# Performance work log

Measured on AMD Instinct MI355X. Metric: run time of the kernel, lower is better.

The kernel has to match this reference:

```python
import jax, jax.numpy as jnp
import numpy as np

EMBED_DIM = 1024
NUM_HEADS = 16
HEAD_DIM = EMBED_DIM // NUM_HEADS
STD = 0.02


def setup_inputs() -> dict:
    key = jax.random.key(0)
    k1, k2, k3 = jax.random.split(key, 3)
    B, S = 2, 2048
    inputs = jax.random.normal(k1, (B, S, EMBED_DIM), dtype=jnp.float32)
    # qkv projection: Linear(E, 3E); torch Linear weight is [out, in]
    w_qkv = jax.random.normal(k2, (3 * EMBED_DIM, EMBED_DIM), dtype=jnp.float32) * STD
    b_qkv = jnp.zeros((3 * EMBED_DIM,), dtype=jnp.float32)
    w_out = jax.random.normal(k3, (EMBED_DIM, EMBED_DIM), dtype=jnp.float32) * STD
    b_out = jnp.zeros((EMBED_DIM,), dtype=jnp.float32)
    return {"inputs": inputs, "w_qkv": w_qkv, "b_qkv": b_qkv, "w_out": w_out, "b_out": b_out}


def reference(inputs, w_qkv, b_qkv, w_out, b_out):
    B, S, E = inputs.shape
    qkv = inputs @ w_qkv.T + b_qkv                      # [B,S,3E]
    q, k, v = jnp.split(qkv, 3, axis=2)                 # each [B,S,E]

    def split_heads(t):
        return t.reshape(B, S, NUM_HEADS, HEAD_DIM).transpose(0, 2, 1, 3)  # [B,H,S,D]

    q, k, v = split_heads(q), split_heads(k), split_heads(v)
    scores = jnp.einsum('bhqd,bhkd->bhqk', q, k) * (1.0 / np.sqrt(HEAD_DIM))
    causal = jnp.tril(jnp.ones((S, S), dtype=bool))     # [S,S]
    scores = jnp.where(causal[None, None, :, :], scores, -jnp.inf)
    probs = jax.nn.softmax(scores, axis=-1)             # dropout is identity in eval mode
    ctx = jnp.einsum('bhqk,bhkd->bhqd', probs, v)       # [B,H,S,D]
    ctx = ctx.transpose(0, 2, 1, 3).reshape(B, S, E)
    return ctx @ w_out.T + b_out
```

## Files before the change

kernel.cpp:

```cpp
#include <hip/hip_runtime.h>
#include <hip/hip_bf16.h>

#define BATCH 2
#define SEQ   2048
#define EMB   1024
#define NHEAD 16
#define HDIM  64
#define MTOT  (BATCH*SEQ)
#define KTOT  EMB

#define NX  (MTOT*EMB)
#define NW1 (3*EMB*EMB)
#define NW2 (EMB*EMB)
#define NCVT (NX+NW1+NW2)

typedef short bf8 __attribute__((ext_vector_type(8)));
typedef short s4v __attribute__((ext_vector_type(4)));
typedef float f4  __attribute__((ext_vector_type(4)));
typedef unsigned int uint;

__device__ __forceinline__ short f2b(float f) {
    __hip_bfloat16 h = __float2bfloat16(f);
    return __builtin_bit_cast(short, h);
}
__device__ __forceinline__ void gl_lds16(const short* g, short* l) {
    __builtin_amdgcn_global_load_lds(
        (const __attribute__((address_space(1))) uint*)g,
        (__attribute__((address_space(3))) uint*)l, 16, 0, 0);
}
#define SWZ_SRC(lane)      ((((lane) ^ ((lane)>>2) ^ ((lane)>>4)) & 3) * 8)
#define SWZ_RD(quad, l16)  ((((quad) ^ (l16) ^ ((l16)>>2)) & 3) * 8)

__global__ __launch_bounds__(256) void cvt_all(
    const float* __restrict__ X, const float* __restrict__ W1,
    const float* __restrict__ W2,
    short* __restrict__ xb, short* __restrict__ w1b, short* __restrict__ w2b)
{
    int i4 = (blockIdx.x * 256 + threadIdx.x) * 4;
    const float* src; short* dst; int off;
    if (i4 < NX)            { src = X;  dst = xb;  off = i4; }
    else if (i4 < NX + NW1) { src = W1; dst = w1b; off = i4 - NX; }
    else                    { src = W2; dst = w2b; off = i4 - NX - NW1; }
    float4 v = *(const float4*)&src[off];
    s4v o; o[0]=f2b(v.x); o[1]=f2b(v.y); o[2]=f2b(v.z); o[3]=f2b(v.w);
    *(s4v*)&dst[off] = o;
}

__global__ __launch_bounds__(256) void gemm_qkv(
    const short* __restrict__ Xb, const short* __restrict__ Wb,
    const float* __restrict__ bias,
    short* __restrict__ qb, short* __restrict__ kb, short* __restrict__ vtb)
{
    __shared__ __align__(16) short As[2*128*32];
    __shared__ __align__(16) short Bs[2*128*32];
    const int tid  = threadIdx.x;
    const int lane = tid & 63;
    const int w    = tid >> 6;
    const int l16  = lane & 15, quad = lane >> 4;
    const int wm   = (w >> 1) * 64, wn = (w & 1) * 64;
    const int srow = (lane >> 2);
    const int scol = SWZ_SRC(lane);
    f4 acc[4][4] = {};
    for (int k0 = 0; k0 < KTOT; k0 += 64) {
        #pragma unroll
        for (int t = 0; t < 4; t++) {
            const int rr = w*32 + (t & 1)*16;
            const int kc = t >> 1;
            int ra = blockIdx.x*128 + rr + srow;
            gl_lds16(&Xb[(size_t)ra*KTOT + k0 + kc*32 + scol], &As[kc*4096 + rr*32]);
            int rb = blockIdx.y*128 + rr + srow;
            gl_lds16(&Wb[(size_t)rb*KTOT + k0 + kc*32 + scol], &Bs[kc*4096 + rr*32]);
        }
        __syncthreads();
        #pragma unroll
        for (int kc = 0; kc < 2; kc++) {
            bf8 af[4], bf[4];
            #pragma unroll
            for (int t = 0; t < 4; t++) {
                af[t] = *(const bf8*)&As[kc*4096 + (wm + t*16 + l16)*32 + SWZ_RD(quad, l16)];
                bf[t] = *(const bf8*)&Bs[kc*4096 + (wn + t*16 + l16)*32 + SWZ_RD(quad, l16)];
            }
            #pragma unroll
            for (int mt = 0; mt < 4; mt++)
                #pragma unroll
                for (int nt = 0; nt < 4; nt++)
                    acc[mt][nt] = __builtin_amdgcn_mfma_f32_16x16x32_bf16(af[mt], bf[nt], acc[mt][nt], 0, 0, 0);
        }
        __syncthreads();
    }
    #pragma unroll
    for (int mt = 0; mt < 4; mt++)
    #pragma unroll
    for (int nt = 0; nt < 4; nt++) {
        int colg = blockIdx.y*128 + wn + nt*16 + l16;
        float bv = bias[colg];
        #pragma unroll
        for (int r = 0; r < 4; r++) {
            int rowg = blockIdx.x*128 + wm + mt*16 + quad*4 + r;
            short h = f2b(acc[mt][nt][r] + bv);
            int bb = rowg >> 11, s = rowg & 2047;
            if (colg < 1024) {
                int hh = colg >> 6, d = colg & 63;
                qb[(((bb*NHEAD + hh)*SEQ + s) << 6) + d] = h;
            } else if (colg < 2048) {
                int c2 = colg - 1024, hh = c2 >> 6, d = c2 & 63;
                kb[(((bb*NHEAD + hh)*SEQ + s) << 6) + d] = h;
            } else {
                int c3 = colg - 2048, hh = c3 >> 6, d = c3 & 63;
                int ssw = (s & ~63) | (((s & 15) << 2) | ((s >> 4) & 3));
                vtb[((bb*NHEAD + hh)*HDIM + d)*SEQ + ssw] = h;
            }
        }
    }
}

__global__ __launch_bounds__(256, 4) void attn(
    const short* __restrict__ qb, const short* __restrict__ kb,
    const short* __restrict__ vtb, short* __restrict__ ctx)
{
    __shared__ __align__(16) short Ks[2*4096];
    __shared__ __align__(16) short Vs[2*4096];
    __shared__ __align__(16) short pl[4][16*64];
    const int tid = threadIdx.x;
    const int w = tid >> 6, lane = tid & 63;
    const int l16 = lane & 15, quad = lane >> 4;
    const int f  = blockIdx.x;
    const int bh = f & 31;
    const int j5 = (f >> 5) & 7;
    const int hq = f >> 8;
    const int tq = (hq == 0) ? j5 : (hq == 1) ? (15 - j5)
                 : (hq == 2) ? (16 + j5) : (31 - j5);
    const int q0w = tq*64 + w*16;
    const int base = bh * (SEQ*HDIM);
    short* myp = pl[w];
    const float SC = 0.125f * 1.44269504f;

    const int lq  = lane >> 2;
    const int lsw = SWZ_SRC(lane);

    const bool isk = (w < 2);
    short* tb = isk ? Ks : Vs;
    const int sstep = isk ? 64*HDIM : 64;
    const short* sp0; const short* sp1; const short* sp2; const short* sp3;
    int dof[4];
    {
        const int wb2 = (w & 1) * 4;
        #pragma unroll
        for (int tt = 0; tt < 4; tt++) {
            int t = wb2 + tt, cc = t & 1, g = (t >> 1) & 3;
            dof[tt] = (cc*64 + g*16)*32;
            const short* s = isk ? &kb[base + (g*16 + lq)*HDIM + cc*32 + lsw]
                                 : &vtb[base + (g*16 + lq)*SEQ + cc*32 + lsw];
            if (tt == 0) sp0 = s; else if (tt == 1) sp1 = s;
            else if (tt == 2) sp2 = s; else sp3 = s;
        }
    }

    bf8 qa[2];
    #pragma unroll
    for (int kc = 0; kc < 2; kc++)
        qa[kc] = *(const bf8*)&qb[base + (q0w + l16)*HDIM + kc*32 + quad*8];

    f4 o[4] = {};
    float lacc[4] = {};
    const int rdK = l16*32 + SWZ_RD(quad, l16);

    gl_lds16(sp0, tb + dof[0]); gl_lds16(sp1, tb + dof[1]);
    gl_lds16(sp2, tb + dof[2]); gl_lds16(sp3, tb + dof[3]);
    sp0 += sstep; sp1 += sstep; sp2 += sstep; sp3 += sstep;
    __syncthreads();

    int buf = 0;
    for (int st = 0; st <= tq; st++) {
        if (st < tq) {
            short* d = tb + (buf ^ 1)*4096;
            gl_lds16(sp0, d + dof[0]); gl_lds16(sp1, d + dof[1]);
            gl_lds16(sp2, d + dof[2]); gl_lds16(sp3, d + dof[3]);
            sp0 += sstep; sp1 += sstep; sp2 += sstep; sp3 += sstep;
        }
        const int kbase = buf*4096 + rdK;
        f4 s[4] = {};
        #pragma unroll
        for (int kf = 0; kf < 4; kf++)
            #pragma unroll
            for (int c = 0; c < 2; c++) {
                bf8 kfr = *(const bf8*)&Ks[kbase + (c*64 + kf*16)*32];
                s[kf] = __builtin_amdgcn_mfma_f32_16x16x32_bf16(qa[c], kfr, s[kf], 0, 0, 0);
            }
        if (st == tq) {
            const int j0 = st*64;
            #pragma unroll
            for (int r = 0; r < 4; r++) {
                const int row = quad*4 + r;
                const int qi  = q0w + row;
                float e[4];
                #pragma unroll
                for (int kf = 0; kf < 4; kf++) {
                    e[kf] = __builtin_amdgcn_exp2f(s[kf][r] * SC);
                    if (j0 + kf*16 + l16 > qi) e[kf] = 0.0f;
                    lacc[r] += e[kf];
                }
                uint u01 = __builtin_amdgcn_perm(__builtin_bit_cast(uint, e[1]),
                                                 __builtin_bit_cast(uint, e[0]), 0x07060302u);
                uint u23 = __builtin_amdgcn_perm(__builtin_bit_cast(uint, e[3]),
                                                 __builtin_bit_cast(uint, e[2]), 0x07060302u);
                uint2 pk = {u01, u23};
                int c8 = ((l16 >> 1) ^ (row & 7));
                *(uint2*)&myp[row*64 + c8*8 + (l16 & 1)*4] = pk;
            }
        } else {
            #pragma unroll
            for (int r = 0; r < 4; r++) {
                const int row = quad*4 + r;
                float e[4];
                #pragma unroll
                for (int kf = 0; kf < 4; kf++) {
                    e[kf] = __builtin_amdgcn_exp2f(s[kf][r] * SC);
                    lacc[r] += e[kf];
                }
                uint u01 = __builtin_amdgcn_perm(__builtin_bit_cast(uint, e[1]),
                                                 __builtin_bit_cast(uint, e[0]), 0x07060302u);
                uint u23 = __builtin_amdgcn_perm(__builtin_bit_cast(uint, e[3]),
                                                 __builtin_bit_cast(uint, e[2]), 0x07060302u);
                uint2 pk = {u01, u23};
                int c8 = ((l16 >> 1) ^ (row & 7));
                *(uint2*)&myp[row*64 + c8*8 + (l16 & 1)*4] = pk;
            }
        }
        asm volatile("" ::: "memory");
        bf8 pa[2];
        #pragma unroll
        for (int kc = 0; kc < 2; kc++)
            pa[kc] = *(const bf8*)&myp[l16*64 + (((kc*4 + quad) ^ (l16 & 7)))*8];
        #pragma unroll
        for (int dt = 0; dt < 4; dt++)
            #pragma unroll
            for (int c = 0; c < 2; c++) {
                bf8 vf = *(const bf8*)&Vs[kbase + (c*64 + dt*16)*32];
                o[dt] = __builtin_amdgcn_mfma_f32_16x16x32_bf16(pa[c], vf, o[dt], 0, 0, 0);
            }
        __syncthreads();
        buf ^= 1;
    }
    #pragma unroll
    for (int r = 0; r < 4; r++) {
        float v = lacc[r];
        v += __shfl_xor(v, 1);
        v += __shfl_xor(v, 2);
        v += __shfl_xor(v, 4);
        v += __shfl_xor(v, 8);
        lacc[r] = v;
    }
    const int b = bh >> 4, h = bh & 15;
    #pragma unroll
    for (int r = 0; r < 4; r++) {
        float inv = 1.0f / lacc[r];
        int qi = q0w + quad*4 + r;
        int rowoff = (b*SEQ + qi)*EMB + h*HDIM;
        #pragma unroll
        for (int dt = 0; dt < 4; dt++)
            ctx[rowoff + dt*16 + l16] = f2b(o[dt][r] * inv);
    }
}

__global__ __launch_bounds__(256) void gemm_out(
    const short* __restrict__ A, const short* __restrict__ Wb,
    const float* __restrict__ bias, float* __restrict__ out)
{
    __shared__ __align__(16) short As[2*64*32];
    __shared__ __align__(16) short Bs[2*64*32];
    const int f = blockIdx.x;
    const int xcd = f & 7, i = f >> 3;
    const int by = xcd*2 + (i & 1);
    const int bx = i >> 1;
    const int tid  = threadIdx.x;
    const int lane = tid & 63;
    const int w    = tid >> 6;
    const int l16  = lane & 15, quad = lane >> 4;
    const int wm   = (w >> 1) * 32, wn = (w & 1) * 32;
    const int srow = (lane >> 2);
    const int scol = SWZ_SRC(lane);
    f4 acc[2][2] = {};
    for (int k0 = 0; k0 < KTOT; k0 += 64) {
        #pragma unroll
        for (int kc = 0; kc < 2; kc++) {
            int ra = bx*64 + w*16 + srow;
            gl_lds16(&A[(size_t)ra*KTOT + k0 + kc*32 + scol],  &As[kc*2048 + (w*16)*32]);
            int rb = by*64 + w*16 + srow;
            gl_lds16(&Wb[(size_t)rb*KTOT + k0 + kc*32 + scol], &Bs[kc*2048 + (w*16)*32]);
        }
        __syncthreads();
        #pragma unroll
        for (int kc = 0; kc < 2; kc++) {
            bf8 af[2], bf[2];
            #pragma unroll
            for (int t = 0; t < 2; t++) {
                af[t] = *(const bf8*)&As[kc*2048 + (wm + t*16 + l16)*32 + SWZ_RD(quad, l16)];
                bf[t] = *(const bf8*)&Bs[kc*2048 + (wn + t*16 + l16)*32 + SWZ_RD(quad, l16)];
            }
            #pragma unroll
            for (int mt = 0; mt < 2; mt++)
                #pragma unroll
                for (int nt = 0; nt < 2; nt++)
                    acc[mt][nt] = __builtin_amdgcn_mfma_f32_16x16x32_bf16(af[mt], bf[nt], acc[mt][nt], 0, 0, 0);
        }
        __syncthreads();
    }
    #pragma unroll
    for (int mt = 0; mt < 2; mt++)
    #pragma unroll
    for (int nt = 0; nt < 2; nt++) {
        int colg = by*64 + wn + nt*16 + l16;
        float bv = bias[colg];
        #pragma unroll
        for (int r = 0; r < 4; r++) {
            int rowg = bx*64 + wm + mt*16 + quad*4 + r;
            out[(size_t)rowg*EMB + colg] = acc[mt][nt][r] + bv;
        }
    }
}

extern "C" void kernel_launch(void* const* d_in, const int* in_sizes, int n_in,
                              void* d_out, int out_size, void* d_ws, size_t ws_size,
                              hipStream_t stream) {
    const float* X    = (const float*)d_in[0];
    const float* Wqkv = (const float*)d_in[1];
    const float* Bqkv = (const float*)d_in[2];
    const float* Wout = (const float*)d_in[3];
    const float* Bout = (const float*)d_in[4];
    float* out = (float*)d_out;

    short* xb    = (short*)d_ws;
    short* w1b   = xb  + NX;
    short* w2b   = w1b + NW1;
    short* qb    = w2b + NW2;
    short* kb    = qb  + NX;
    short* vtb   = kb  + NX;
    short* ctx   = vtb + NX;

    cvt_all<<<NCVT/1024, 256, 0, stream>>>(X, Wqkv, Wout, xb, w1b, w2b);
    dim3 g1(MTOT/128, 3*EMB/128);
    gemm_qkv<<<g1, 256, 0, stream>>>(xb, w1b, Bqkv, qb, kb, vtb);
    attn<<<dim3(1024), 256, 0, stream>>>(qb, kb, vtb, ctx);
    gemm_out<<<dim3(1024), 256, 0, stream>>>(ctx, w2b, Bout, out);
}
```

Measured before the change: 176.8 us.

## Double-buffer LDS in both GEMMs and retile QKV GEMM to 256x192 blocks

Both projection GEMMs now double-buffer their LDS tiles. The next K-slice's global-to-LDS loads are issued before computing on the current slice, and one barrier per iteration is removed. The QKV GEMM grows from 128x128 tiles with 256 threads to 256x192 tiles with 512 threads and 8x3 MFMA accumulators per wave, launched as a 1D grid of 256 blocks with an XCD-aware block remap. This aims to hide load latency and raise data reuse, at the cost of more LDS and registers per block and a grid that may fill the CUs unevenly.

```diff
diff --git a/kernel.cpp b/kernel.cpp
--- a/kernel.cpp
+++ b/kernel.cpp
@@ -46,69 +46,101 @@
     *(s4v*)&dst[off] = o;
 }
 
-__global__ __launch_bounds__(256) void gemm_qkv(
+__global__ __launch_bounds__(512, 2) void gemm_qkv(
     const short* __restrict__ Xb, const short* __restrict__ Wb,
     const float* __restrict__ bias,
     short* __restrict__ qb, short* __restrict__ kb, short* __restrict__ vtb)
 {
-    __shared__ __align__(16) short As[2*128*32];
-    __shared__ __align__(16) short Bs[2*128*32];
+    __shared__ __align__(16) short As[2*2*256*32];
+    __shared__ __align__(16) short Bs[2*2*192*32];
     const int tid  = threadIdx.x;
     const int lane = tid & 63;
     const int w    = tid >> 6;
     const int l16  = lane & 15, quad = lane >> 4;
-    const int wm   = (w >> 1) * 64, wn = (w & 1) * 64;
-    const int srow = (lane >> 2);
+    const int wm   = (w >> 2) * 128;
+    const int wn   = (w & 3) * 48;
+    const int srow = lane >> 2;
     const int scol = SWZ_SRC(lane);
-    f4 acc[4][4] = {};
-    for (int k0 = 0; k0 < KTOT; k0 += 64) {
-        #pragma unroll
-        for (int t = 0; t < 4; t++) {
-            const int rr = w*32 + (t & 1)*16;
-            const int kc = t >> 1;
-            int ra = blockIdx.x*128 + rr + srow;
-            gl_lds16(&Xb[(size_t)ra*KTOT + k0 + kc*32 + scol], &As[kc*4096 + rr*32]);
-            int rb = blockIdx.y*128 + rr + srow;
-            gl_lds16(&Wb[(size_t)rb*KTOT + k0 + kc*32 + scol], &Bs[kc*4096 + rr*32]);
+
+    const int id  = blockIdx.x;
+    const int sid = (id & 7) * 32 + (id >> 3);
+    const int bm  = sid >> 4, bn = sid & 15;
+    const int row0 = bm * 256, col0 = bn * 192;
+
+    const short* pa[4]; int da[4];
+    #pragma unroll
+    for (int j = 0; j < 4; j++) {
+        int idx = j*8 + w, kc = idx & 1, g = idx >> 1;
+        pa[j] = &Xb[(size_t)(row0 + g*16 + srow)*KTOT + kc*32 + scol];
+        da[j] = (kc*256 + g*16) * 32;
+    }
+    const short* pb[3]; int db[3];
+    #pragma unroll
+    for (int j = 0; j < 3; j++) {
+        int idx = j*8 + w, kc = idx & 1, g = idx >> 1;
+        pb[j] = &Wb[(size_t)(col0 + g*16 + srow)*KTOT + kc*32 + scol];
+        db[j] = (kc*192 + g*16) * 32;
+    }
+
+    f4 acc[8][3] = {};
+
+    #pragma unroll
+    for (int j = 0; j < 4; j++) gl_lds16(pa[j], &As[da[j]]);
+    #pragma unroll
+    for (int j = 0; j < 3; j++) gl_lds16(pb[j], &Bs[db[j]]);
+    __syncthreads();
+
+    for (int t = 0; t < 16; t++) {
+        const int buf = t & 1;
+        if (t < 15) {
+            const int boA = (buf ^ 1) * 16384;
+            const int boB = (buf ^ 1) * 12288;
+            const int ko  = (t + 1) * 64;
+            #pragma unroll
+            for (int j = 0; j < 4; j++) gl_lds16(pa[j] + ko, &As[boA + da[j]]);
+            #pragma unroll
+            for (int j = 0; j < 3; j++) gl_lds16(pb[j] + ko, &Bs[boB + db[j]]);
+        }
+        const int ab = buf * 16384, bb = buf * 12288;
+        #pragma unroll
+        for (int kc = 0; kc < 2; kc++) {
+            bf8 af[8], bf[3];
+            #pragma unroll
+            for (int m = 0; m < 8; m++)
+                af[m] = *(const bf8*)&As[ab + (kc*256 + wm + m*16 + l16)*32 + SWZ_RD(quad, l16)];
+            #pragma unroll
+            for (int n = 0; n < 3; n++)
+                bf[n] = *(const bf8*)&Bs[bb + (kc*192 + wn + n*16 + l16)*32 + SWZ_RD(quad, l16)];
+            #pragma unroll
+            for (int m = 0; m < 8; m++)
+                #pragma unroll
+                for (int n = 0; n < 3; n++)
+                    acc[m][n] = __builtin_amdgcn_mfma_f32_16x16x32_bf16(af[m], bf[n], acc[m][n], 0, 0, 0);
         }
         __syncthreads();
-        #pragma unroll
-        for (int kc = 0; kc < 2; kc++) {
-            bf8 af[4], bf[4];
-            #pragma unroll
-            for (int t = 0; t < 4; t++) {
-                af[t] = *(const bf8*)&As[kc*4096 + (wm + t*16 + l16)*32 + SWZ_RD(quad, l16)];
-                bf[t] = *(const bf8*)&Bs[kc*4096 + (wn + t*16 + l16)*32 + SWZ_RD(quad, l16)];
-            }
-            #pragma unroll
-            for (int mt = 0; mt < 4; mt++)
-                #pragma unroll
-                for (int nt = 0; nt < 4; nt++)
-                    acc[mt][nt] = __builtin_amdgcn_mfma_f32_16x16x32_bf16(af[mt], bf[nt], acc[mt][nt], 0, 0, 0);
-        }
-        __syncthreads();
-    }
-    #pragma unroll
-    for (int mt = 0; mt < 4; mt++)
-    #pragma unroll
-    for (int nt = 0; nt < 4; nt++) {
-        int colg = blockIdx.y*128 + wn + nt*16 + l16;
+    }
+
+    #pragma unroll
+    for (int m = 0; m < 8; m++)
+    #pragma unroll
+    for (int n = 0; n < 3; n++) {
+        int colg = col0 + wn + n*16 + l16;
         float bv = bias[colg];
         #pragma unroll
         for (int r = 0; r < 4; r++) {
-            int rowg = blockIdx.x*128 + wm + mt*16 + quad*4 + r;
-            short h = f2b(acc[mt][nt][r] + bv);
-            int bb = rowg >> 11, s = rowg & 2047;
+            int rowg = row0 + wm + m*16 + quad*4 + r;
+            short h = f2b(acc[m][n][r] + bv);
+            int bb2 = rowg >> 11, s = rowg & 2047;
             if (colg < 1024) {
                 int hh = colg >> 6, d = colg & 63;
-                qb[(((bb*NHEAD + hh)*SEQ + s) << 6) + d] = h;
+                qb[(((bb2*NHEAD + hh)*SEQ + s) << 6) + d] = h;
             } else if (colg < 2048) {
                 int c2 = colg - 1024, hh = c2 >> 6, d = c2 & 63;
-                kb[(((bb*NHEAD + hh)*SEQ + s) << 6) + d] = h;
+                kb[(((bb2*NHEAD + hh)*SEQ + s) << 6) + d] = h;
             } else {
                 int c3 = colg - 2048, hh = c3 >> 6, d = c3 & 63;
                 int ssw = (s & ~63) | (((s & 15) << 2) | ((s >> 4) & 3));
-                vtb[((bb*NHEAD + hh)*HDIM + d)*SEQ + ssw] = h;
+                vtb[((bb2*NHEAD + hh)*HDIM + d)*SEQ + ssw] = h;
             }
         }
     }
@@ -267,8 +299,8 @@
     const short* __restrict__ A, const short* __restrict__ Wb,
     const float* __restrict__ bias, float* __restrict__ out)
 {
-    __shared__ __align__(16) short As[2*64*32];
-    __shared__ __align__(16) short Bs[2*64*32];
+    __shared__ __align__(16) short As[2*2*64*32];
+    __shared__ __align__(16) short Bs[2*2*64*32];
     const int f = blockIdx.x;
     const int xcd = f & 7, i = f >> 3;
     const int by = xcd*2 + (i & 1);
@@ -280,23 +312,35 @@
     const int wm   = (w >> 1) * 32, wn = (w & 1) * 32;
     const int srow = (lane >> 2);
     const int scol = SWZ_SRC(lane);
+
+    const short* pa0 = &A [(size_t)(bx*64 + w*16 + srow)*KTOT + 0*32 + scol];
+    const short* pa1 = &A [(size_t)(bx*64 + w*16 + srow)*KTOT + 1*32 + scol];
+    const short* pb0 = &Wb[(size_t)(by*64 + w*16 + srow)*KTOT + 0*32 + scol];
+    const short* pb1 = &Wb[(size_t)(by*64 + w*16 + srow)*KTOT + 1*32 + scol];
+    const int d0 = (0*64 + w*16)*32, d1 = (1*64 + w*16)*32;
+
     f4 acc[2][2] = {};
-    for (int k0 = 0; k0 < KTOT; k0 += 64) {
-        #pragma unroll
-        for (int kc = 0; kc < 2; kc++) {
-            int ra = bx*64 + w*16 + srow;
-            gl_lds16(&A[(size_t)ra*KTOT + k0 + kc*32 + scol],  &As[kc*2048 + (w*16)*32]);
-            int rb = by*64 + w*16 + srow;
-            gl_lds16(&Wb[(size_t)rb*KTOT + k0 + kc*32 + scol], &Bs[kc*2048 + (w*16)*32]);
-        }
-        __syncthreads();
+
+    gl_lds16(pa0, &As[d0]); gl_lds16(pa1, &As[d1]);
+    gl_lds16(pb0, &Bs[d0]); gl_lds16(pb1, &Bs[d1]);
+    __syncthreads();
+
+    for (int t = 0; t < 16; t++) {
+        const int buf = t & 1;
+        if (t < 15) {
+            const int bo = (buf ^ 1) * 4096;
+            const int ko = (t + 1) * 64;
+            gl_lds16(pa0 + ko, &As[bo + d0]); gl_lds16(pa1 + ko, &As[bo + d1]);
+            gl_lds16(pb0 + ko, &Bs[bo + d0]); gl_lds16(pb1 + ko, &Bs[bo + d1]);
+        }
+        const int ab = buf * 4096;
         #pragma unroll
         for (int kc = 0; kc < 2; kc++) {
             bf8 af[2], bf[2];
             #pragma unroll
-            for (int t = 0; t < 2; t++) {
-                af[t] = *(const bf8*)&As[kc*2048 + (wm + t*16 + l16)*32 + SWZ_RD(quad, l16)];
-                bf[t] = *(const bf8*)&Bs[kc*2048 + (wn + t*16 + l16)*32 + SWZ_RD(quad, l16)];
+            for (int t2 = 0; t2 < 2; t2++) {
+                af[t2] = *(const bf8*)&As[ab + (kc*64 + wm + t2*16 + l16)*32 + SWZ_RD(quad, l16)];
+                bf[t2] = *(const bf8*)&Bs[ab + (kc*64 + wn + t2*16 + l16)*32 + SWZ_RD(quad, l16)];
             }
             #pragma unroll
             for (int mt = 0; mt < 2; mt++)
@@ -306,6 +350,7 @@
         }
         __syncthreads();
     }
+
     #pragma unroll
     for (int mt = 0; mt < 2; mt++)
     #pragma unroll
@@ -339,8 +384,7 @@
     short* ctx   = vtb + NX;
 
     cvt_all<<<NCVT/1024, 256, 0, stream>>>(X, Wqkv, Wout, xb, w1b, w2b);
-    dim3 g1(MTOT/128, 3*EMB/128);
-    gemm_qkv<<<g1, 256, 0, stream>>>(xb, w1b, Bqkv, qb, kb, vtb);
+    gemm_qkv<<<dim3(256), 512, 0, stream>>>(xb, w1b, Bqkv, qb, kb, vtb);
     attn<<<dim3(1024), 256, 0, stream>>>(qb, kb, vtb, ctx);
     gemm_out<<<dim3(1024), 256, 0, stream>>>(ctx, w2b, Bout, out);
 }
```

Result: slower. 190.7 us (+7.9%).

## Rewrite QKV GEMM as 256x256 tile, 8-wave double-buffered pipelined kernel

Applied to the files above, without the earlier changes.

The QKV projection GEMM moves from 128x128 tiles with 4 waves and a plain load-sync-compute loop to 256x256 tiles with 8 waves. Shared memory is double-buffered, and global-to-LDS loads for the next k-step are interleaved with four MFMA quadrants, using explicit vmcnt waits, raw barriers and s_setprio around the MFMA bursts. Block ids are remapped into groups so neighbouring blocks share rows and columns for L2 reuse. The aim is to hide memory latency and raise arithmetic intensity, at the cost of fewer blocks (192), higher register pressure and fragile hand-tuned waitcnt ordering.

```diff
diff --git a/kernel.cpp b/kernel.cpp
--- a/kernel.cpp
+++ b/kernel.cpp
@@ -30,6 +30,10 @@
 }
 #define SWZ_SRC(lane)      ((((lane) ^ ((lane)>>2) ^ ((lane)>>4)) & 3) * 8)
 #define SWZ_RD(quad, l16)  ((((quad) ^ (l16) ^ ((l16)>>2)) & 3) * 8)
+
+#define BARRIER() do { asm volatile("" ::: "memory"); \
+                       __builtin_amdgcn_s_barrier(); \
+                       asm volatile("" ::: "memory"); } while (0)
 
 __global__ __launch_bounds__(256) void cvt_all(
     const float* __restrict__ X, const float* __restrict__ W1,
@@ -46,69 +50,168 @@
     *(s4v*)&dst[off] = o;
 }
 
-__global__ __launch_bounds__(256) void gemm_qkv(
+__global__ __launch_bounds__(512, 1) void gemm_qkv(
     const short* __restrict__ Xb, const short* __restrict__ Wb,
     const float* __restrict__ bias,
     short* __restrict__ qb, short* __restrict__ kb, short* __restrict__ vtb)
 {
-    __shared__ __align__(16) short As[2*128*32];
-    __shared__ __align__(16) short Bs[2*128*32];
+    __shared__ __align__(16) short As[2*2*256*32];
+    __shared__ __align__(16) short Bs[2*2*256*32];
     const int tid  = threadIdx.x;
     const int lane = tid & 63;
     const int w    = tid >> 6;
     const int l16  = lane & 15, quad = lane >> 4;
-    const int wm   = (w >> 1) * 64, wn = (w & 1) * 64;
-    const int srow = (lane >> 2);
+    const int wh   = w >> 2;
+    const int wl   = w & 3;
+    const int wm   = wh * 128;
+    const int wn   = wl * 64;
+    const int srow = lane >> 2;
     const int scol = SWZ_SRC(lane);
-    f4 acc[4][4] = {};
-    for (int k0 = 0; k0 < KTOT; k0 += 64) {
-        #pragma unroll
-        for (int t = 0; t < 4; t++) {
-            const int rr = w*32 + (t & 1)*16;
-            const int kc = t >> 1;
-            int ra = blockIdx.x*128 + rr + srow;
-            gl_lds16(&Xb[(size_t)ra*KTOT + k0 + kc*32 + scol], &As[kc*4096 + rr*32]);
-            int rb = blockIdx.y*128 + rr + srow;
-            gl_lds16(&Wb[(size_t)rb*KTOT + k0 + kc*32 + scol], &Bs[kc*4096 + rr*32]);
-        }
-        __syncthreads();
+
+    const int id  = blockIdx.x;
+    const int x   = id & 7;
+    const int j   = id >> 3;
+    const int bmL = j / 6, bnL = j - bmL*6;
+    const int bm  = (x & 3)*4 + bmL;
+    const int bn  = (x >> 2)*6 + bnL;
+    const int row0 = bm * 256, col0 = bn * 256;
+
+    const short* pA0[2]; const short* pA1[2];
+    const short* pB0[2]; const short* pB1[2];
+    int dA0[2], dA1[2], dB0[2], dB1[2];
+    #pragma unroll
+    for (int kc = 0; kc < 2; kc++) {
+        int ra0 = wm + 0  + wl*16;
+        int ra1 = wm + 64 + wl*16;
+        int rb0 = wn + 0  + wh*16;
+        int rb1 = wn + 32 + wh*16;
+        pA0[kc] = &Xb[(size_t)(row0 + ra0 + srow)*KTOT + kc*32 + scol];
+        pA1[kc] = &Xb[(size_t)(row0 + ra1 + srow)*KTOT + kc*32 + scol];
+        pB0[kc] = &Wb[(size_t)(col0 + rb0 + srow)*KTOT + kc*32 + scol];
+        pB1[kc] = &Wb[(size_t)(col0 + rb1 + srow)*KTOT + kc*32 + scol];
+        dA0[kc] = kc*8192 + ra0*32;
+        dA1[kc] = kc*8192 + ra1*32;
+        dB0[kc] = kc*8192 + rb0*32;
+        dB1[kc] = kc*8192 + rb1*32;
+    }
+
+    f4 acc[8][4] = {};
+
+    gl_lds16(pA0[0], &As[dA0[0]]); gl_lds16(pA0[1], &As[dA0[1]]);
+    gl_lds16(pB0[0], &Bs[dB0[0]]); gl_lds16(pB0[1], &Bs[dB0[1]]);
+    gl_lds16(pB1[0], &Bs[dB1[0]]); gl_lds16(pB1[1], &Bs[dB1[1]]);
+    gl_lds16(pA1[0], &As[dA1[0]]); gl_lds16(pA1[1], &As[dA1[1]]);
+    asm volatile("s_waitcnt vmcnt(4)" ::: "memory");
+    BARRIER();
+
+    const int swz = SWZ_RD(quad, l16);
+    bf8 af[4][2], bf0[2][2], bf1[2][2];
+
+    for (int t = 0; t < 16; t++) {
+        const int ab = (t & 1) * 16384;
+        const int nb = ((t & 1) ^ 1) * 16384;
+        const int ko = (t + 1) * 64;
+
         #pragma unroll
         for (int kc = 0; kc < 2; kc++) {
-            bf8 af[4], bf[4];
-            #pragma unroll
-            for (int t = 0; t < 4; t++) {
-                af[t] = *(const bf8*)&As[kc*4096 + (wm + t*16 + l16)*32 + SWZ_RD(quad, l16)];
-                bf[t] = *(const bf8*)&Bs[kc*4096 + (wn + t*16 + l16)*32 + SWZ_RD(quad, l16)];
-            }
-            #pragma unroll
-            for (int mt = 0; mt < 4; mt++)
-                #pragma unroll
-                for (int nt = 0; nt < 4; nt++)
-                    acc[mt][nt] = __builtin_amdgcn_mfma_f32_16x16x32_bf16(af[mt], bf[nt], acc[mt][nt], 0, 0, 0);
-        }
-        __syncthreads();
-    }
-    #pragma unroll
-    for (int mt = 0; mt < 4; mt++)
-    #pragma unroll
-    for (int nt = 0; nt < 4; nt++) {
-        int colg = blockIdx.y*128 + wn + nt*16 + l16;
+            #pragma unroll
+            for (int m = 0; m < 4; m++)
+                af[m][kc] = *(const bf8*)&As[ab + kc*8192 + (wm + m*16 + l16)*32 + swz];
+            #pragma unroll
+            for (int n = 0; n < 2; n++)
+                bf0[n][kc] = *(const bf8*)&Bs[ab + kc*8192 + (wn + n*16 + l16)*32 + swz];
+        }
+        gl_lds16(pA0[0] + ko, &As[nb + dA0[0]]);
+        gl_lds16(pA0[1] + ko, &As[nb + dA0[1]]);
+        asm volatile("s_waitcnt vmcnt(4)" ::: "memory");
+        BARRIER();
+        __builtin_amdgcn_s_setprio(1);
+        #pragma unroll
+        for (int m = 0; m < 4; m++)
+            #pragma unroll
+            for (int n = 0; n < 2; n++)
+                #pragma unroll
+                for (int kc = 0; kc < 2; kc++)
+                    acc[m][n] = __builtin_amdgcn_mfma_f32_16x16x32_bf16(af[m][kc], bf0[n][kc], acc[m][n], 0, 0, 0);
+        __builtin_amdgcn_s_setprio(0);
+        BARRIER();
+
+        #pragma unroll
+        for (int kc = 0; kc < 2; kc++)
+            #pragma unroll
+            for (int n = 0; n < 2; n++)
+                bf1[n][kc] = *(const bf8*)&Bs[ab + kc*8192 + (wn + 32 + n*16 + l16)*32 + swz];
+        gl_lds16(pB0[0] + ko, &Bs[nb + dB0[0]]);
+        gl_lds16(pB0[1] + ko, &Bs[nb + dB0[1]]);
+        asm volatile("s_waitcnt vmcnt(4)" ::: "memory");
+        BARRIER();
+        __builtin_amdgcn_s_setprio(1);
+        #pragma unroll
+        for (int m = 0; m < 4; m++)
+            #pragma unroll
+            for (int n = 0; n < 2; n++)
+                #pragma unroll
+                for (int kc = 0; kc < 2; kc++)
+                    acc[m][2+n] = __builtin_amdgcn_mfma_f32_16x16x32_bf16(af[m][kc], bf1[n][kc], acc[m][2+n], 0, 0, 0);
+        __builtin_amdgcn_s_setprio(0);
+        BARRIER();
+
+        #pragma unroll
+        for (int kc = 0; kc < 2; kc++)
+            #pragma unroll
+            for (int m = 0; m < 4; m++)
+                af[m][kc] = *(const bf8*)&As[ab + kc*8192 + (wm + 64 + m*16 + l16)*32 + swz];
+        gl_lds16(pB1[0] + ko, &Bs[nb + dB1[0]]);
+        gl_lds16(pB1[1] + ko, &Bs[nb + dB1[1]]);
+        BARRIER();
+        __builtin_amdgcn_s_setprio(1);
+        #pragma unroll
+        for (int m = 0; m < 4; m++)
+            #pragma unroll
+            for (int n = 0; n < 2; n++)
+                #pragma unroll
+                for (int kc = 0; kc < 2; kc++)
+                    acc[4+m][2+n] = __builtin_amdgcn_mfma_f32_16x16x32_bf16(af[m][kc], bf1[n][kc], acc[4+m][2+n], 0, 0, 0);
+        __builtin_amdgcn_s_setprio(0);
+        BARRIER();
+
+        gl_lds16(pA1[0] + ko, &As[nb + dA1[0]]);
+        gl_lds16(pA1[1] + ko, &As[nb + dA1[1]]);
+        asm volatile("s_waitcnt vmcnt(4)" ::: "memory");
+        BARRIER();
+        __builtin_amdgcn_s_setprio(1);
+        #pragma unroll
+        for (int m = 0; m < 4; m++)
+            #pragma unroll
+            for (int n = 0; n < 2; n++)
+                #pragma unroll
+                for (int kc = 0; kc < 2; kc++)
+                    acc[4+m][n] = __builtin_amdgcn_mfma_f32_16x16x32_bf16(af[m][kc], bf0[n][kc], acc[4+m][n], 0, 0, 0);
+        __builtin_amdgcn_s_setprio(0);
+        BARRIER();
+    }
+
+    #pragma unroll
+    for (int m = 0; m < 8; m++)
+    #pragma unroll
+    for (int n = 0; n < 4; n++) {
+        int colg = col0 + wn + n*16 + l16;
         float bv = bias[colg];
         #pragma unroll
         for (int r = 0; r < 4; r++) {
-            int rowg = blockIdx.x*128 + wm + mt*16 + quad*4 + r;
-            short h = f2b(acc[mt][nt][r] + bv);
-            int bb = rowg >> 11, s = rowg & 2047;
+            int rowg = row0 + wm + m*16 + quad*4 + r;
+            short h = f2b(acc[m][n][r] + bv);
+            int bb2 = rowg >> 11, s = rowg & 2047;
             if (colg < 1024) {
                 int hh = colg >> 6, d = colg & 63;
-                qb[(((bb*NHEAD + hh)*SEQ + s) << 6) + d] = h;
+                qb[(((bb2*NHEAD + hh)*SEQ + s) << 6) + d] = h;
             } else if (colg < 2048) {
                 int c2 = colg - 1024, hh = c2 >> 6, d = c2 & 63;
-                kb[(((bb*NHEAD + hh)*SEQ + s) << 6) + d] = h;
+                kb[(((bb2*NHEAD + hh)*SEQ + s) << 6) + d] = h;
             } else {
                 int c3 = colg - 2048, hh = c3 >> 6, d = c3 & 63;
                 int ssw = (s & ~63) | (((s & 15) << 2) | ((s >> 4) & 3));
-                vtb[((bb*NHEAD + hh)*HDIM + d)*SEQ + ssw] = h;
+                vtb[((bb2*NHEAD + hh)*HDIM + d)*SEQ + ssw] = h;
             }
         }
     }
@@ -339,8 +442,7 @@
     short* ctx   = vtb + NX;
 
     cvt_all<<<NCVT/1024, 256, 0, stream>>>(X, Wqkv, Wout, xb, w1b, w2b);
-    dim3 g1(MTOT/128, 3*EMB/128);
-    gemm_qkv<<<g1, 256, 0, stream>>>(xb, w1b, Bqkv, qb, kb, vtb);
+    gemm_qkv<<<dim3(192), 512, 0, stream>>>(xb, w1b, Bqkv, qb, kb, vtb);
     attn<<<dim3(1024), 256, 0, stream>>>(qb, kb, vtb, ctx);
     gemm_out<<<dim3(1024), 256, 0, stream>>>(ctx, w2b, Bout, out);
 }
```

Result: slower. 200.9 us (+13.6%).
